# Kernel tuning notes

Hardware: AMD Instinct MI355X
Metric: run time of the kernel (lower is better)

Reference implementation:

```python
import jax, jax.numpy as jnp
import numpy as np

DIM = 384
NUM_HEADS = 6
HEAD_DIM = DIM // NUM_HEADS
MLP_HIDDEN = 4 * DIM
SCALE = HEAD_DIM ** -0.5
EPS = 1e-5


def layer_norm(x, w, b):
    mu = jnp.mean(x, axis=-1, keepdims=True)
    var = jnp.mean(jnp.square(x - mu), axis=-1, keepdims=True)
    return (x - mu) * jax.lax.rsqrt(var + EPS) * w + b


def setup_inputs() -> dict:
    key = jax.random.key(0)
    ks = jax.random.split(key, 24)
    d = DIM
    s = 0.02
    inp = {
        'x1': jax.random.normal(ks[0], (16, d, 32, 32), jnp.float32),
        'x2': jax.random.normal(ks[1], (16, d, 32, 32), jnp.float32),
        # per-branch attention-input LayerNorm + kqv projection (no bias)
        'ln_a1_w': jnp.ones((d,), jnp.float32), 'ln_a1_b': jnp.zeros((d,), jnp.float32),
        'kqv1_w': jax.random.normal(ks[2], (d, 3 * d), jnp.float32) * s,
        'ln_a2_w': jnp.ones((d,), jnp.float32), 'ln_a2_b': jnp.zeros((d,), jnp.float32),
        'kqv2_w': jax.random.normal(ks[3], (d, 3 * d), jnp.float32) * s,
        # output projections
        'proj1_w': jax.random.normal(ks[4], (d, d), jnp.float32) * s,
        'proj1_b': jnp.zeros((d,), jnp.float32),
        'proj2_w': jax.random.normal(ks[5], (d, d), jnp.float32) * s,
        'proj2_b': jnp.zeros((d,), jnp.float32),
        # post-attention LayerNorms
        'ln1_w': jnp.ones((d,), jnp.float32), 'ln1_b': jnp.zeros((d,), jnp.float32),
        'ln2_w': jnp.ones((d,), jnp.float32), 'ln2_b': jnp.zeros((d,), jnp.float32),
        # MLPs
        'mlp1_fc1_w': jax.random.normal(ks[6], (d, MLP_HIDDEN), jnp.float32) * s,
        'mlp1_fc1_b': jnp.zeros((MLP_HIDDEN,), jnp.float32),
        'mlp1_fc2_w': jax.random.normal(ks[7], (MLP_HIDDEN, d), jnp.float32) * s,
        'mlp1_fc2_b': jnp.zeros((d,), jnp.float32),
        'mlp2_fc1_w': jax.random.normal(ks[8], (d, MLP_HIDDEN), jnp.float32) * s,
        'mlp2_fc1_b': jnp.zeros((MLP_HIDDEN,), jnp.float32),
        'mlp2_fc2_w': jax.random.normal(ks[9], (MLP_HIDDEN, d), jnp.float32) * s,
        'mlp2_fc2_b': jnp.zeros((d,), jnp.float32),
    }
    return inp


def _kqv_branch(x, ln_w, ln_b, Wkqv):
    # x: [B, C, H, W] -> embedding [B, N, C]; k,q,v: [B, h, N, hd]
    B, C, H, W = x.shape
    N = H * W
    emb = x.reshape(B, C, N).transpose(0, 2, 1)
    xn = layer_norm(emb, ln_w, ln_b)
    kqv = (xn @ Wkqv).reshape(B, N, 3, NUM_HEADS, HEAD_DIM).transpose(2, 0, 3, 1, 4)
    return kqv[0], kqv[1], kqv[2], emb


def _cross_attn(q, k, v):
    # q,k,v: [B, h, N, hd] -> [B, N, C]
    scores = jnp.einsum('bhnd,bhmd->bhnm', q, k) * SCALE
    a = jax.nn.softmax(scores, axis=-1)
    o = jnp.einsum('bhnm,bhmd->bhnd', a, v)
    B, h, N, hd = o.shape
    return o.transpose(0, 2, 1, 3).reshape(B, N, h * hd)


def reference(x1, x2, ln_a1_w, ln_a1_b, kqv1_w, ln_a2_w, ln_a2_b, kqv2_w,
              proj1_w, proj1_b, proj2_w, proj2_b, ln1_w, ln1_b, ln2_w, ln2_b,
              mlp1_fc1_w, mlp1_fc1_b, mlp1_fc2_w, mlp1_fc2_b,
              mlp2_fc1_w, mlp2_fc1_b, mlp2_fc2_w, mlp2_fc2_b):
    B, C, H, W = x1.shape
    k1, q1, v1, emb1 = _kqv_branch(x1, ln_a1_w, ln_a1_b, kqv1_w)
    k2, q2, v2, emb2 = _kqv_branch(x2, ln_a2_w, ln_a2_b, kqv2_w)
    a1 = _cross_attn(q1, k2, v2)   # branch 1 queries attend to branch 2
    a2 = _cross_attn(q2, k1, v1)
    out1 = emb1 + (a1 @ proj1_w + proj1_b)
    h1 = layer_norm(out1, ln1_w, ln1_b)
    out1 = out1 + (jax.nn.gelu(h1 @ mlp1_fc1_w + mlp1_fc1_b, approximate=False) @ mlp1_fc2_w + mlp1_fc2_b)
    out2 = emb2 + (a2 @ proj2_w + proj2_b)
    h2 = layer_norm(out2, ln2_w, ln2_b)
    out2 = out2 + (jax.nn.gelu(h2 @ mlp2_fc1_w + mlp2_fc1_b, approximate=False) @ mlp2_fc2_w + mlp2_fc2_b)
    out1 = out1.transpose(0, 2, 1).reshape(B, C, H, W)
    out2 = out2.transpose(0, 2, 1).reshape(B, C, H, W)
    return (out1, out2)
```

## Files before the change

kernel.cpp:

```cpp
#include <hip/hip_runtime.h>
#include <math.h>

typedef unsigned short u16;
typedef __attribute__((ext_vector_type(8))) short short8;
typedef __attribute__((ext_vector_type(4))) float f32x4;

#define MFMA(a,b,c) __builtin_amdgcn_mfma_f32_16x16x32_bf16(a, b, c, 0, 0, 0)
#define SWZ(row, ch) ((((ch) ^ ((row) & 7)) << 3))
#define EXP2F(x) __builtin_amdgcn_exp2f(x)

__device__ __forceinline__ float b2f(u16 v) {
    union { unsigned int i; float f; } c; c.i = ((unsigned int)v) << 16; return c.f;
}
__device__ __forceinline__ u16 f2b(float f) {
    union { float f; unsigned int i; } c; c.f = f;
    unsigned int u = c.i;
    return (u16)((u + 0x7fffu + ((u >> 16) & 1u)) >> 16);
}
__device__ __forceinline__ u16 f2b_p(float f) {
    union { float f; unsigned int i; } c; c.f = f;
    return (u16)((c.i + 0x8000u) >> 16);
}

struct TWArgs { const float* src[8]; u16* dst[8]; int K[8]; int N[8]; };

__global__ __launch_bounds__(256) void transpose_w(TWArgs a) {
    int wi = blockIdx.z;
    int K = a.K[wi], N = a.N[wi];
    int n0 = blockIdx.x * 32, k0 = blockIdx.y * 32;
    if (n0 >= N || k0 >= K) return;
    __shared__ float t[32][33];
    const float* s = a.src[wi]; u16* d = a.dst[wi];
    int tx = threadIdx.x & 31, ty = threadIdx.x >> 5;
    for (int i = 0; i < 32; i += 8)
        t[ty + i][tx] = s[(size_t)(k0 + ty + i) * N + n0 + tx];
    __syncthreads();
    for (int i = 0; i < 32; i += 8)
        d[(size_t)(n0 + ty + i) * K + k0 + tx] = f2b(t[tx][ty + i]);
}

__global__ __launch_bounds__(256)
void ln_tr(const float* __restrict__ x0, const float* __restrict__ x1,
           const float* __restrict__ w0, const float* __restrict__ bb0,
           const float* __restrict__ w1, const float* __restrict__ bb1,
           u16* __restrict__ xn0, u16* __restrict__ xn1) {
    int br = blockIdx.z;
    const float* x  = br ? x1 : x0;
    const float* wv = br ? w1 : w0;
    const float* bv = br ? bb1 : bb0;
    u16* xn = br ? xn1 : xn0;
    int b = blockIdx.y, n0 = blockIdx.x * 32;
    __shared__ float tile[32][385];
    __shared__ float smu[32], srs[32];
    int tid = threadIdx.x;
    const float* xb = x + (size_t)b * 384 * 1024 + n0;
    for (int idx = tid; idx < 384 * 32; idx += 256) {
        int c = idx >> 5, nn = idx & 31;
        tile[nn][c] = xb[(size_t)c * 1024 + nn];
    }
    __syncthreads();
    {
        int nn = tid >> 3, part = tid & 7;
        float s1 = 0.f, s2 = 0.f;
        for (int c = part * 48; c < part * 48 + 48; ++c) {
            float v = tile[nn][c]; s1 += v; s2 += v * v;
        }
        for (int off = 1; off < 8; off <<= 1) {
            s1 += __shfl_xor(s1, off, 64); s2 += __shfl_xor(s2, off, 64);
        }
        if (part == 0) {
            float mu = s1 * (1.f / 384.f);
            float var = s2 * (1.f / 384.f) - mu * mu;
            smu[nn] = mu; srs[nn] = rsqrtf(fmaxf(var, 0.f) + 1e-5f);
        }
    }
    __syncthreads();
    size_t rowbase = (size_t)b * 1024 + n0;
    for (int idx = tid; idx < 32 * 384; idx += 256) {
        int nn = idx / 384, c = idx - nn * 384;
        float v = tile[nn][c];
        float g = (v - smu[nn]) * srs[nn] * wv[c] + bv[c];
        xn[(rowbase + nn) * 384 + c] = f2b(g);
    }
}

__global__ __launch_bounds__(256)
void ln_rows(const float* __restrict__ i0, const float* __restrict__ i1,
             const float* __restrict__ w0, const float* __restrict__ bb0,
             const float* __restrict__ w1, const float* __restrict__ bb1,
             u16* __restrict__ o0, u16* __restrict__ o1) {
    int br = blockIdx.z;
    const float* in = br ? i1 : i0;
    const float* wv = br ? w1 : w0;
    const float* bv = br ? bb1 : bb0;
    u16* out = br ? o1 : o0;
    int w = threadIdx.x >> 6, l = threadIdx.x & 63;
    size_t row = (size_t)blockIdx.x * 4 + w;
    const float* p = in + row * 384;
    float v[6]; float s1 = 0.f, s2 = 0.f;
    #pragma unroll
    for (int j = 0; j < 6; j++) { v[j] = p[j * 64 + l]; s1 += v[j]; s2 += v[j] * v[j]; }
    for (int off = 1; off < 64; off <<= 1) {
        s1 += __shfl_xor(s1, off, 64); s2 += __shfl_xor(s2, off, 64);
    }
    float mu = s1 * (1.f / 384.f);
    float var = s2 * (1.f / 384.f) - mu * mu;
    float rs = rsqrtf(fmaxf(var, 0.f) + 1e-5f);
    #pragma unroll
    for (int j = 0; j < 6; j++) {
        int c = j * 64 + l;
        out[row * 384 + c] = f2b((v[j] - mu) * rs * wv[c] + bv[c]);
    }
}

template <int EPI>
__global__ __launch_bounds__(256)
void gemm128(const u16* __restrict__ A0, const u16* __restrict__ A1,
             const u16* __restrict__ B0, const u16* __restrict__ B1,
             void* C0v, void* C1v,
             const float* __restrict__ bias0, const float* __restrict__ bias1,
             const void* R0v, const void* R1v,
             int N, int K) {
    const int br = blockIdx.z;
    const u16* A = br ? A1 : A0;
    const u16* B = br ? B1 : B0;
    void* Cv = br ? C1v : C0v;
    const float* bias = br ? bias1 : bias0;
    const void* Rv = br ? R1v : R0v;

    const int n0 = blockIdx.x * 128;
    const int m0 = blockIdx.y * 128;
    const int tid = threadIdx.x;
    const int w = tid >> 6, l = tid & 63;
    const int wm = w >> 1, wn = w & 1;
    const int lr = l & 15, lq = l >> 4;

    __shared__ alignas(16) u16 As[2][128 * 40];
    __shared__ alignas(16) u16 Bs[2][128 * 40];

    f32x4 acc[4][4];
    #pragma unroll
    for (int i = 0; i < 4; i++)
        #pragma unroll
        for (int j = 0; j < 4; j++) acc[i][j] = (f32x4)0.0f;

    const int ar0 = tid >> 2, ac0 = (tid & 3) * 8;
    const int ar1 = ar0 + 64;
    const u16* Ap0 = A + (size_t)(m0 + ar0) * K + ac0;
    const u16* Ap1 = A + (size_t)(m0 + ar1) * K + ac0;
    const u16* Bp0 = B + (size_t)(n0 + ar0) * K + ac0;
    const u16* Bp1 = B + (size_t)(n0 + ar1) * K + ac0;

    const int nk = K >> 5;
    uint4 pa0 = *(const uint4*)Ap0, pa1 = *(const uint4*)Ap1;
    uint4 pb0 = *(const uint4*)Bp0, pb1 = *(const uint4*)Bp1;
    *(uint4*)&As[0][ar0 * 40 + ac0] = pa0;
    *(uint4*)&As[0][ar1 * 40 + ac0] = pa1;
    *(uint4*)&Bs[0][ar0 * 40 + ac0] = pb0;
    *(uint4*)&Bs[0][ar1 * 40 + ac0] = pb1;
    pa0 = *(const uint4*)(Ap0 + 32); pa1 = *(const uint4*)(Ap1 + 32);
    pb0 = *(const uint4*)(Bp0 + 32); pb1 = *(const uint4*)(Bp1 + 32);
    __syncthreads();

    for (int kt = 0; kt < nk; ++kt) {
        const int cur = kt & 1;
        if (kt + 1 < nk) {
            const int nx = cur ^ 1;
            *(uint4*)&As[nx][ar0 * 40 + ac0] = pa0;
            *(uint4*)&As[nx][ar1 * 40 + ac0] = pa1;
            *(uint4*)&Bs[nx][ar0 * 40 + ac0] = pb0;
            *(uint4*)&Bs[nx][ar1 * 40 + ac0] = pb1;
        }
        if (kt + 2 < nk) {
            const int kb = (kt + 2) * 32;
            pa0 = *(const uint4*)(Ap0 + kb); pa1 = *(const uint4*)(Ap1 + kb);
            pb0 = *(const uint4*)(Bp0 + kb); pb1 = *(const uint4*)(Bp1 + kb);
        }
        short8 af[4], bf[4];
        #pragma unroll
        for (int mt = 0; mt < 4; ++mt)
            af[mt] = *(const short8*)&As[cur][(wm * 64 + mt * 16 + lr) * 40 + lq * 8];
        #pragma unroll
        for (int nt = 0; nt < 4; ++nt)
            bf[nt] = *(const short8*)&Bs[cur][(wn * 64 + nt * 16 + lr) * 40 + lq * 8];
        #pragma unroll
        for (int mt = 0; mt < 4; ++mt)
            #pragma unroll
            for (int nt = 0; nt < 4; ++nt)
                acc[mt][nt] = MFMA(af[mt], bf[nt], acc[mt][nt]);
        __syncthreads();
    }

    #pragma unroll
    for (int mt = 0; mt < 4; ++mt)
        #pragma unroll
        for (int nt = 0; nt < 4; ++nt) {
            const int col = n0 + wn * 64 + nt * 16 + lr;
            const int rbase = m0 + wm * 64 + mt * 16 + lq * 4;
            const float bv = (EPI == 0) ? 0.f : bias[col];
            #pragma unroll
            for (int r = 0; r < 4; r++) {
                const int row = rbase + r;
                const size_t idx = (size_t)row * N + col;
                float v = acc[mt][nt][r];
                if (EPI == 0) {
                    if (col < 768) {
                        ((u16*)Cv)[idx] = f2b(col >= 384 ? v * 0.18033688f : v);
                    } else {
                        u16* vtb = (u16*)Rv;
                        vtb[((((size_t)(row >> 10)) * 6 + ((col - 768) >> 6)) * 64
                             + (col & 63)) * 1024 + (row & 1023)] = f2b(v);
                    }
                } else if (EPI == 1) {
                    float xr = ((const float*)Rv)[
                        ((size_t)(row >> 10) * 384 + col) * 1024 + (row & 1023)];
                    ((float*)Cv)[idx] = v + bv + xr;
                } else if (EPI == 2) {
                    v += bv;
                    float g = 0.5f * v * (1.f + erff(v * 0.70710678118f));
                    ((u16*)Cv)[idx] = f2b(g);
                } else {
                    ((float*)Cv)[idx] = v + bv + ((const float*)Rv)[idx];
                }
            }
        }
}

__global__ __launch_bounds__(256)
void attn_k(const u16* __restrict__ kqvA, const u16* __restrict__ kqvB,
            const u16* __restrict__ vtA, const u16* __restrict__ vtB,
            u16* __restrict__ oA, u16* __restrict__ oB) {
    const int bid = blockIdx.x;
    const int g = bid & 7, qb = (bid >> 3) & 7, s = bid >> 6;
    const int grp = s * 8 + g;
    const int ob = grp & 1, h = (grp >> 1) % 6, b = grp / 12;

    const u16* kqvQ  = (ob ? kqvB : kqvA) + (size_t)b * 1024 * 1152;
    const u16* kqvKV = (ob ? kqvA : kqvB) + (size_t)b * 1024 * 1152;
    const u16* vt    = (ob ? vtA : vtB) + ((size_t)b * 6 + h) * 64 * 1024;
    u16* outp = (ob ? oB : oA) + (size_t)b * 1024 * 384;
    const u16* qp = kqvQ + 384 + h * 64;
    const u16* kp = kqvKV + h * 64;

    __shared__ alignas(16) u16 Ks[2][64 * 64];
    __shared__ alignas(16) u16 Vts[2][64 * 64];
    __shared__ alignas(16) u16 Ps[4 * 32 * 64];

    const int tid = threadIdx.x, w = tid >> 6, l = tid & 63;
    const int lr = l & 15, lq = l >> 4;
    u16* Psw = Ps + w * 32 * 64;

    short8 qf[2][2];
    #pragma unroll
    for (int a = 0; a < 2; a++)
        #pragma unroll
        for (int ks = 0; ks < 2; ks++)
            qf[a][ks] = *(const short8*)&qp[
                (size_t)(qb * 128 + w * 32 + a * 16 + lr) * 1152 + ks * 32 + lq * 8];

    const int srow = tid >> 3, sch = tid & 7;
    uint4 kpre[2][2], vpre[2][2];
    #pragma unroll
    for (int t = 0; t < 2; t++)
        #pragma unroll
        for (int i = 0; i < 2; i++) {
            int row = srow + i * 32;
            kpre[t][i] = *(const uint4*)&kp[(size_t)(t * 64 + row) * 1152 + sch * 8];
            vpre[t][i] = *(const uint4*)&vt[(size_t)row * 1024 + t * 64 + sch * 8];
        }

    #pragma unroll
    for (int i = 0; i < 2; i++) {
        int row = srow + i * 32;
        int o = row * 64 + SWZ(row, sch);
        *(uint4*)&Ks[0][o] = kpre[0][i];
        *(uint4*)&Vts[0][o] = vpre[0][i];
    }
    #pragma unroll
    for (int i = 0; i < 2; i++) {
        int row = srow + i * 32;
        kpre[0][i] = *(const uint4*)&kp[(size_t)(2 * 64 + row) * 1152 + sch * 8];
        vpre[0][i] = *(const uint4*)&vt[(size_t)row * 1024 + 2 * 64 + sch * 8];
    }

    f32x4 oacc[2][4];
    float psum[2][4];
    #pragma unroll
    for (int a = 0; a < 2; a++)
        #pragma unroll
        for (int n = 0; n < 4; n++) oacc[a][n] = (f32x4)0.0f;
    #pragma unroll
    for (int a = 0; a < 2; a++)
        #pragma unroll
        for (int r = 0; r < 4; r++) psum[a][r] = 0.f;

    __syncthreads();

    for (int jt = 0; jt < 16; ++jt) {
        const int cur = jt & 1, nx = cur ^ 1;
        if (jt + 1 < 16) {
            #pragma unroll
            for (int i = 0; i < 2; i++) {
                int row = srow + i * 32;
                int o = row * 64 + SWZ(row, sch);
                *(uint4*)&Ks[nx][o] = kpre[nx][i];
                *(uint4*)&Vts[nx][o] = vpre[nx][i];
            }
            if (jt + 3 < 16) {
                #pragma unroll
                for (int i = 0; i < 2; i++) {
                    int row = srow + i * 32;
                    kpre[nx][i] = *(const uint4*)&kp[(size_t)((jt + 3) * 64 + row) * 1152 + sch * 8];
                    vpre[nx][i] = *(const uint4*)&vt[(size_t)row * 1024 + (jt + 3) * 64 + sch * 8];
                }
            }
        }

        f32x4 sacc[2][4];
        #pragma unroll
        for (int a = 0; a < 2; a++)
            #pragma unroll
            for (int n = 0; n < 4; n++) sacc[a][n] = (f32x4)0.0f;
        __builtin_amdgcn_s_setprio(1);
        #pragma unroll
        for (int ks = 0; ks < 2; ++ks) {
            short8 bk[4];
            #pragma unroll
            for (int n = 0; n < 4; n++) {
                int row = n * 16 + lr;
                bk[n] = *(const short8*)&Ks[cur][row * 64 + SWZ(row, ks * 4 + lq)];
            }
            #pragma unroll
            for (int a = 0; a < 2; a++)
                #pragma unroll
                for (int n = 0; n < 4; n++) sacc[a][n] = MFMA(qf[a][ks], bk[n], sacc[a][n]);
        }
        __builtin_amdgcn_s_setprio(0);

        #pragma unroll
        for (int a = 0; a < 2; a++)
            #pragma unroll
            for (int r = 0; r < 4; r++) {
                int prow = a * 16 + lq * 4 + r;
                float ps = 0.f;
                #pragma unroll
                for (int n = 0; n < 4; n++) {
                    float p = EXP2F(sacc[a][n][r]);
                    ps += p;
                    Psw[prow * 64 + ((((2 * n + (lr >> 3)) ^ (prow & 7)) << 3) + (lr & 7))] = f2b_p(p);
                }
                psum[a][r] += ps;
            }

        __builtin_amdgcn_s_setprio(1);
        #pragma unroll
        for (int ks = 0; ks < 2; ++ks) {
            short8 ap[2], bv4[4];
            #pragma unroll
            for (int a = 0; a < 2; a++) {
                int row = a * 16 + lr;
                ap[a] = *(const short8*)&Psw[row * 64 + SWZ(row, ks * 4 + lq)];
            }
            #pragma unroll
            for (int n = 0; n < 4; n++) {
                int row = n * 16 + lr;
                bv4[n] = *(const short8*)&Vts[cur][row * 64 + SWZ(row, ks * 4 + lq)];
            }
            #pragma unroll
            for (int a = 0; a < 2; a++)
                #pragma unroll
                for (int n = 0; n < 4; n++) oacc[a][n] = MFMA(ap[a], bv4[n], oacc[a][n]);
        }
        __builtin_amdgcn_s_setprio(0);
        __syncthreads();
    }

    #pragma unroll
    for (int a = 0; a < 2; a++)
        #pragma unroll
        for (int r = 0; r < 4; r++) {
            float sm = psum[a][r];
            sm += __shfl_xor(sm, 1, 64); sm += __shfl_xor(sm, 2, 64);
            sm += __shfl_xor(sm, 4, 64); sm += __shfl_xor(sm, 8, 64);
            psum[a][r] = 1.f / sm;
        }
    #pragma unroll
    for (int a = 0; a < 2; a++)
        #pragma unroll
        for (int n = 0; n < 4; n++)
            #pragma unroll
            for (int r = 0; r < 4; r++) {
                size_t row = (size_t)qb * 128 + w * 32 + a * 16 + lq * 4 + r;
                int col = h * 64 + n * 16 + lr;
                outp[row * 384 + col] = f2b(oacc[a][n][r] * psum[a][r]);
            }
}

__global__ __launch_bounds__(256)
void transpose_out(const float* __restrict__ r0, const float* __restrict__ r1,
                   float* __restrict__ out) {
    int z = blockIdx.z, ob = z >> 4, b = z & 15;
    const float* rp = ob ? r1 : r0;
    int c0 = blockIdx.y * 32, n0 = blockIdx.x * 32;
    __shared__ float t[32][33];
    int tx = threadIdx.x & 31, ty = threadIdx.x >> 5;
    for (int i = 0; i < 32; i += 8)
        t[ty + i][tx] = rp[((size_t)b * 1024 + n0 + ty + i) * 384 + c0 + tx];
    __syncthreads();
    for (int i = 0; i < 32; i += 8)
        out[(size_t)ob * 6291456 + ((size_t)b * 384 + c0 + ty + i) * 1024 + n0 + tx]
            = t[tx][ty + i];
}

extern "C" void kernel_launch(void* const* d_in, const int* in_sizes, int n_in,
                              void* d_out, int out_size, void* d_ws, size_t ws_size,
                              hipStream_t stream) {
    const float* x1      = (const float*)d_in[0];
    const float* x2      = (const float*)d_in[1];
    const float* ln_a1_w = (const float*)d_in[2];
    const float* ln_a1_b = (const float*)d_in[3];
    const float* kqv1_w  = (const float*)d_in[4];
    const float* ln_a2_w = (const float*)d_in[5];
    const float* ln_a2_b = (const float*)d_in[6];
    const float* kqv2_w  = (const float*)d_in[7];
    const float* proj1_w = (const float*)d_in[8];
    const float* proj1_b = (const float*)d_in[9];
    const float* proj2_w = (const float*)d_in[10];
    const float* proj2_b = (const float*)d_in[11];
    const float* ln1_w   = (const float*)d_in[12];
    const float* ln1_b   = (const float*)d_in[13];
    const float* ln2_w   = (const float*)d_in[14];
    const float* ln2_b   = (const float*)d_in[15];
    const float* m1f1w   = (const float*)d_in[16];
    const float* m1f1b   = (const float*)d_in[17];
    const float* m1f2w   = (const float*)d_in[18];
    const float* m1f2b   = (const float*)d_in[19];
    const float* m2f1w   = (const float*)d_in[20];
    const float* m2f1b   = (const float*)d_in[21];
    const float* m2f2w   = (const float*)d_in[22];
    const float* m2f2b   = (const float*)d_in[23];
    (void)in_sizes; (void)n_in; (void)out_size; (void)ws_size;

    const size_t R = 16384;
    char* ws = (char*)d_ws;
    size_t off = 0;
    auto alloc = [&](size_t bytes) -> char* {
        char* p = ws + off;
        off = (off + bytes + 255) & ~(size_t)255;
        return p;
    };
    u16* kqv1t  = (u16*)alloc(1152 * 384 * 2);
    u16* kqv2t  = (u16*)alloc(1152 * 384 * 2);
    u16* proj1t = (u16*)alloc(384 * 384 * 2);
    u16* proj2t = (u16*)alloc(384 * 384 * 2);
    u16* fc11t  = (u16*)alloc(1536 * 384 * 2);
    u16* fc12t  = (u16*)alloc(1536 * 384 * 2);
    u16* fc21t  = (u16*)alloc(384 * 1536 * 2);
    u16* fc22t  = (u16*)alloc(384 * 1536 * 2);
    u16* xn1 = (u16*)alloc(R * 384 * 2);
    u16* xn2 = (u16*)alloc(R * 384 * 2);
    char* regC = alloc(R * 1152 * 2 * 2);
    u16* kqv1 = (u16*)regC;
    u16* kqv2 = (u16*)(regC + R * 1152 * 2);
    float* oa1 = (float*)regC;
    float* oa2 = (float*)(regC + R * 384 * 4);
    u16* hid_b2 = (u16*)(regC + 2 * R * 384 * 4);
    u16* at1 = (u16*)d_out;
    u16* at2 = at1 + R * 384;
    u16* vt1 = at2 + R * 384;
    u16* vt2 = vt1 + (size_t)16 * 6 * 64 * 1024;
    u16* hid_b1 = (u16*)d_out;

    TWArgs tw;
    tw.src[0] = kqv1_w;  tw.dst[0] = kqv1t;  tw.K[0] = 384;  tw.N[0] = 1152;
    tw.src[1] = kqv2_w;  tw.dst[1] = kqv2t;  tw.K[1] = 384;  tw.N[1] = 1152;
    tw.src[2] = proj1_w; tw.dst[2] = proj1t; tw.K[2] = 384;  tw.N[2] = 384;
    tw.src[3] = proj2_w; tw.dst[3] = proj2t; tw.K[3] = 384;  tw.N[3] = 384;
    tw.src[4] = m1f1w;   tw.dst[4] = fc11t;  tw.K[4] = 384;  tw.N[4] = 1536;
    tw.src[5] = m2f1w;   tw.dst[5] = fc12t;  tw.K[5] = 384;  tw.N[5] = 1536;
    tw.src[6] = m1f2w;   tw.dst[6] = fc21t;  tw.K[6] = 1536; tw.N[6] = 384;
    tw.src[7] = m2f2w;   tw.dst[7] = fc22t;  tw.K[7] = 1536; tw.N[7] = 384;
    transpose_w<<<dim3(48, 48, 8), dim3(256), 0, stream>>>(tw);

    ln_tr<<<dim3(32, 16, 2), dim3(256), 0, stream>>>(
        x1, x2, ln_a1_w, ln_a1_b, ln_a2_w, ln_a2_b, xn1, xn2);

    gemm128<0><<<dim3(9, 128, 2), dim3(256), 0, stream>>>(
        xn1, xn2, kqv1t, kqv2t, (void*)kqv1, (void*)kqv2,
        (const float*)nullptr, (const float*)nullptr,
        (const void*)vt1, (const void*)vt2, 1152, 384);

    attn_k<<<dim3(1536), dim3(256), 0, stream>>>(kqv1, kqv2, vt1, vt2, at1, at2);

    gemm128<1><<<dim3(3, 128, 2), dim3(256), 0, stream>>>(
        at1, at2, proj1t, proj2t, (void*)oa1, (void*)oa2,
        proj1_b, proj2_b, (const void*)x1, (const void*)x2, 384, 384);

    ln_rows<<<dim3(4096, 1, 2), dim3(256), 0, stream>>>(
        oa1, oa2, ln1_w, ln1_b, ln2_w, ln2_b, xn1, xn2);

    for (int half = 0; half < 2; ++half) {
        const size_t ro = (size_t)half * 8192;
        gemm128<2><<<dim3(12, 64, 2), dim3(256), 0, stream>>>(
            xn1 + ro * 384, xn2 + ro * 384, fc11t, fc12t,
            (void*)hid_b1, (void*)hid_b2, m1f1b, m2f1b, nullptr, nullptr, 1536, 384);
        gemm128<3><<<dim3(3, 64, 2), dim3(256), 0, stream>>>(
            hid_b1, hid_b2, fc21t, fc22t,
            (void*)(oa1 + ro * 384), (void*)(oa2 + ro * 384),
            m1f2b, m2f2b, (const void*)(oa1 + ro * 384), (const void*)(oa2 + ro * 384),
            384, 1536);
    }

    transpose_out<<<dim3(32, 12, 32), dim3(256), 0, stream>>>(oa1, oa2, (float*)d_out);
}
```

Baseline: 638.2 us.

## Keep attention probabilities in registers by computing transposed scores and using 16x16x16 MFMA

```diff
diff --git a/kernel.cpp b/kernel.cpp
--- a/kernel.cpp
+++ b/kernel.cpp
@@ -3,11 +3,23 @@
 
 typedef unsigned short u16;
 typedef __attribute__((ext_vector_type(8))) short short8;
+typedef __attribute__((ext_vector_type(4))) short short4b;
 typedef __attribute__((ext_vector_type(4))) float f32x4;
 
 #define MFMA(a,b,c) __builtin_amdgcn_mfma_f32_16x16x32_bf16(a, b, c, 0, 0, 0)
 #define SWZ(row, ch) ((((ch) ^ ((row) & 7)) << 3))
 #define EXP2F(x) __builtin_amdgcn_exp2f(x)
+
+static __device__ __forceinline__ f32x4 MFMA16(short4b a, short4b b, f32x4 c) {
+#if __has_builtin(__builtin_amdgcn_mfma_f32_16x16x16bf16_1k)
+    return __builtin_amdgcn_mfma_f32_16x16x16bf16_1k(a, b, c, 0, 0, 0);
+#else
+    f32x4 d;
+    asm volatile("v_mfma_f32_16x16x16_bf16 %0, %1, %2, %3\n\ts_nop 7"
+                 : "=v"(d) : "v"(a), "v"(b), "v"(c));
+    return d;
+#endif
+}
 
 __device__ __forceinline__ float b2f(u16 v) {
     union { unsigned int i; float f; } c; c.i = ((unsigned int)v) << 16; return c.f;
@@ -244,11 +256,9 @@
 
     __shared__ alignas(16) u16 Ks[2][64 * 64];
     __shared__ alignas(16) u16 Vts[2][64 * 64];
-    __shared__ alignas(16) u16 Ps[4 * 32 * 64];
 
     const int tid = threadIdx.x, w = tid >> 6, l = tid & 63;
     const int lr = l & 15, lq = l >> 4;
-    u16* Psw = Ps + w * 32 * 64;
 
     short8 qf[2][2];
     #pragma unroll
@@ -284,15 +294,11 @@
     }
 
     f32x4 oacc[2][4];
-    float psum[2][4];
+    float psum[2] = {0.f, 0.f};
     #pragma unroll
     for (int a = 0; a < 2; a++)
         #pragma unroll
         for (int n = 0; n < 4; n++) oacc[a][n] = (f32x4)0.0f;
-    #pragma unroll
-    for (int a = 0; a < 2; a++)
-        #pragma unroll
-        for (int r = 0; r < 4; r++) psum[a][r] = 0.f;
 
     __syncthreads();
 
@@ -316,74 +322,76 @@
             }
         }
 
-        f32x4 sacc[2][4];
-        #pragma unroll
-        for (int a = 0; a < 2; a++)
-            #pragma unroll
-            for (int n = 0; n < 4; n++) sacc[a][n] = (f32x4)0.0f;
+        f32x4 sacc[4][2];
+        #pragma unroll
+        for (int kb = 0; kb < 4; kb++)
+            #pragma unroll
+            for (int a = 0; a < 2; a++) sacc[kb][a] = (f32x4)0.0f;
         __builtin_amdgcn_s_setprio(1);
         #pragma unroll
         for (int ks = 0; ks < 2; ++ks) {
             short8 bk[4];
             #pragma unroll
+            for (int kb = 0; kb < 4; kb++) {
+                int row = kb * 16 + lr;
+                bk[kb] = *(const short8*)&Ks[cur][row * 64 + SWZ(row, ks * 4 + lq)];
+            }
+            #pragma unroll
+            for (int kb = 0; kb < 4; kb++)
+                #pragma unroll
+                for (int a = 0; a < 2; a++)
+                    sacc[kb][a] = MFMA(bk[kb], qf[a][ks], sacc[kb][a]);
+        }
+        __builtin_amdgcn_s_setprio(0);
+
+        short4b ap16[2][4];
+        #pragma unroll
+        for (int a = 0; a < 2; a++)
+            #pragma unroll
+            for (int kb = 0; kb < 4; kb++) {
+                f32x4 s4 = sacc[kb][a];
+                float p0 = EXP2F(s4[0]), p1 = EXP2F(s4[1]);
+                float p2 = EXP2F(s4[2]), p3 = EXP2F(s4[3]);
+                psum[a] += (p0 + p1) + (p2 + p3);
+                short4b pk;
+                pk[0] = (short)f2b_p(p0); pk[1] = (short)f2b_p(p1);
+                pk[2] = (short)f2b_p(p2); pk[3] = (short)f2b_p(p3);
+                ap16[a][kb] = pk;
+            }
+
+        __builtin_amdgcn_s_setprio(1);
+        #pragma unroll
+        for (int kb = 0; kb < 4; ++kb) {
+            short4b bv16[4];
+            #pragma unroll
             for (int n = 0; n < 4; n++) {
                 int row = n * 16 + lr;
-                bk[n] = *(const short8*)&Ks[cur][row * 64 + SWZ(row, ks * 4 + lq)];
+                int addr = row * 64 + SWZ(row, kb * 2 + (lq >> 1)) + (lq & 1) * 4;
+                bv16[n] = *(const short4b*)&Vts[cur][addr];
             }
             #pragma unroll
             for (int a = 0; a < 2; a++)
                 #pragma unroll
-                for (int n = 0; n < 4; n++) sacc[a][n] = MFMA(qf[a][ks], bk[n], sacc[a][n]);
-        }
-        __builtin_amdgcn_s_setprio(0);
-
-        #pragma unroll
-        for (int a = 0; a < 2; a++)
-            #pragma unroll
-            for (int r = 0; r < 4; r++) {
-                int prow = a * 16 + lq * 4 + r;
-                float ps = 0.f;
-                #pragma unroll
-                for (int n = 0; n < 4; n++) {
-                    float p = EXP2F(sacc[a][n][r]);
-                    ps += p;
-                    Psw[prow * 64 + ((((2 * n + (lr >> 3)) ^ (prow & 7)) << 3) + (lr & 7))] = f2b_p(p);
-                }
-                psum[a][r] += ps;
-            }
-
-        __builtin_amdgcn_s_setprio(1);
-        #pragma unroll
-        for (int ks = 0; ks < 2; ++ks) {
-            short8 ap[2], bv4[4];
-            #pragma unroll
-            for (int a = 0; a < 2; a++) {
-                int row = a * 16 + lr;
-                ap[a] = *(const short8*)&Psw[row * 64 + SWZ(row, ks * 4 + lq)];
-            }
-            #pragma unroll
-            for (int n = 0; n < 4; n++) {
-                int row = n * 16 + lr;
-                bv4[n] = *(const short8*)&Vts[cur][row * 64 + SWZ(row, ks * 4 + lq)];
-            }
-            #pragma unroll
-            for (int a = 0; a < 2; a++)
-                #pragma unroll
-                for (int n = 0; n < 4; n++) oacc[a][n] = MFMA(ap[a], bv4[n], oacc[a][n]);
+                for (int n = 0; n < 4; n++)
+                    oacc[a][n] = MFMA16(ap16[a][kb], bv16[n], oacc[a][n]);
         }
         __builtin_amdgcn_s_setprio(0);
         __syncthreads();
     }
 
     #pragma unroll
+    for (int a = 0; a < 2; a++) {
+        psum[a] += __shfl_xor(psum[a], 16, 64);
+        psum[a] += __shfl_xor(psum[a], 32, 64);
+        psum[a] = 1.f / psum[a];
+    }
+    float rec[2][4];
+    #pragma unroll
     for (int a = 0; a < 2; a++)
         #pragma unroll
-        for (int r = 0; r < 4; r++) {
-            float sm = psum[a][r];
-            sm += __shfl_xor(sm, 1, 64); sm += __shfl_xor(sm, 2, 64);
-            sm += __shfl_xor(sm, 4, 64); sm += __shfl_xor(sm, 8, 64);
-            psum[a][r] = 1.f / sm;
-        }
+        for (int r = 0; r < 4; r++)
+            rec[a][r] = __shfl(psum[a], lq * 4 + r, 64);
+
     #pragma unroll
     for (int a = 0; a < 2; a++)
         #pragma unroll
@@ -392,7 +400,7 @@
             for (int r = 0; r < 4; r++) {
                 size_t row = (size_t)qb * 128 + w * 32 + a * 16 + lq * 4 + r;
                 int col = h * 64 + n * 16 + lr;
-                outp[row * 384 + col] = f2b(oacc[a][n][r] * psum[a][r]);
+                outp[row * 384 + col] = f2b(oacc[a][n][r] * rec[a][r]);
             }
 }
 
```

Measured after the change: 623.5 us. 2.3% less time.
